# Performance work log

Measured on AMD Instinct MI355X. Metric: run time of the kernel, lower is better.

The kernel has to match this reference:

```python
import jax, jax.numpy as jnp
import numpy as np

B, S, D, H = 4, 2048, 1024, 16
DK = D // H


def setup_inputs() -> dict:
    key = jax.random.key(0)
    ks = jax.random.split(key, 12)
    s = 1.0 / np.sqrt(D)
    return {
        "query": jax.random.normal(ks[0], (B, S, D), jnp.float32),
        "key": jax.random.normal(ks[1], (B, S, D), jnp.float32),
        "value": jax.random.normal(ks[2], (B, S, D), jnp.float32),
        "mask": jax.random.randint(ks[3], (B, S), 0, 2, jnp.int32),
        "wq": jax.random.normal(ks[4], (D, D), jnp.float32) * s,
        "bq": jnp.zeros((D,), jnp.float32),
        "wk": jax.random.normal(ks[5], (D, D), jnp.float32) * s,
        "bk": jnp.zeros((D,), jnp.float32),
        "wv": jax.random.normal(ks[6], (D, D), jnp.float32) * s,
        "bv": jnp.zeros((D,), jnp.float32),
        "wo": jax.random.normal(ks[7], (D, D), jnp.float32) * s,
        "bo": jnp.zeros((D,), jnp.float32),
    }


def reference(query, key, value, mask, wq, bq, wk, bk, wv, bv, wo, bo):
    # torch Linear: y = x @ W.T + b
    def proj(x, w, b):
        y = jnp.einsum('bsd,ed->bse', x, w) + b
        return y.reshape(B, S, H, DK).transpose(0, 2, 1, 3)  # [B,H,S,DK]

    q = proj(query, wq, bq)
    k = proj(key, wk, bk)
    v = proj(value, wv, bv)

    scores = jnp.einsum('bhqd,bhkd->bhqk', q, k) / jnp.sqrt(jnp.float32(DK))
    m = mask[:, None, None, :]  # [B,1,1,S_kv]
    scores = jnp.where(m == 0, jnp.float32(-1e9), scores)
    attn = jax.nn.softmax(scores, axis=-1)  # dropout p=0.0 (eval)
    out = jnp.einsum('bhqk,bhkd->bhqd', attn, v)
    out = out.transpose(0, 2, 1, 3).reshape(B, S, D)
    return jnp.einsum('bsd,ed->bse', out, wo) + bo
```

## Files before the change

kernel.cpp:

```cpp
#include <hip/hip_runtime.h>
#include <hip/hip_bf16.h>

typedef __bf16 bf16;
typedef bf16 bf16x2 __attribute__((ext_vector_type(2)));
typedef bf16 bf16x4 __attribute__((ext_vector_type(4)));
typedef bf16 bf16x8 __attribute__((ext_vector_type(8)));
typedef float f32x4 __attribute__((ext_vector_type(4)));
typedef float f32x16 __attribute__((ext_vector_type(16)));
typedef unsigned int u32;
typedef u32 u32x4 __attribute__((ext_vector_type(4)));

#define MFMA16(A,B,C) __builtin_amdgcn_mfma_f32_16x16x32_bf16(A,B,C,0,0,0)
#define MFMA32(A,B,C) __builtin_amdgcn_mfma_f32_32x32x16_bf16(A,B,C,0,0,0)

__device__ __forceinline__ void gld_lds16(const void* g, void* l) {
  __builtin_amdgcn_global_load_lds(
      (const __attribute__((address_space(1))) void*)g,
      (__attribute__((address_space(3))) void*)l, 16, 0, 0);
}

__global__ void cast3_kernel(const float* __restrict__ s0, const float* __restrict__ s1,
                             const float* __restrict__ s2,
                             bf16* __restrict__ d0, bf16* __restrict__ d1, bf16* __restrict__ d2) {
  const int which = blockIdx.x >> 13;
  const int i = (blockIdx.x & 8191) * 256 + threadIdx.x;
  const float* s = which == 0 ? s0 : which == 1 ? s1 : s2;
  bf16* d = which == 0 ? d0 : which == 1 ? d1 : d2;
  float4 v = ((const float4*)s)[i];
  bf16x4 o;
  o[0] = (bf16)v.x; o[1] = (bf16)v.y; o[2] = (bf16)v.z; o[3] = (bf16)v.w;
  *(bf16x4*)(d + (size_t)i * 4) = o;
}

__global__ void cast4_kernel(const float* __restrict__ s0, const float* __restrict__ s1,
                             const float* __restrict__ s2, const float* __restrict__ s3,
                             bf16* __restrict__ d0, bf16* __restrict__ d1,
                             bf16* __restrict__ d2, bf16* __restrict__ d3) {
  const int which = blockIdx.x >> 10;
  const int i = (blockIdx.x & 1023) * 256 + threadIdx.x;
  const float* s = which == 0 ? s0 : which == 1 ? s1 : which == 2 ? s2 : s3;
  bf16* d = which == 0 ? d0 : which == 1 ? d1 : which == 2 ? d2 : d3;
  float4 v = ((const float4*)s)[i];
  bf16x4 o;
  o[0] = (bf16)v.x; o[1] = (bf16)v.y; o[2] = (bf16)v.z; o[3] = (bf16)v.w;
  *(bf16x4*)(d + (size_t)i * 4) = o;
}

__device__ __forceinline__ void gemm256_core(
    const bf16* __restrict__ aBase, const bf16* __restrict__ bBase,
    bf16* sA, bf16* sB, f32x4 (&acc)[4][4])
{
  const int t = threadIdx.x;
  const int lane = t & 63, w = t >> 6;
  const int wr = w >> 2, wc = w & 3;
  const int c = lane & 15, g = lane >> 4;

  const int pA = t * 16;
  const int lA = pA ^ (((pA >> 7) & 7) << 4);
  const int srA = lA >> 6;
  const int scA = (lA & 63) >> 1;

  auto stage = [&](int buf, int kt) {
    gld_lds16(aBase + (size_t)srA * 1024 + kt * 32 + scA, &sA[buf * 4096 + t * 8]);
#pragma unroll
    for (int r = 0; r < 2; ++r)
      gld_lds16(bBase + (size_t)(r * 128 + srA) * 1024 + kt * 32 + scA,
                &sB[buf * 8192 + r * 4096 + t * 8]);
  };

  auto rd = [&](const bf16* s, int row) -> bf16x8 {
    const int phys = (row * 64 + g * 16) ^ (((row >> 1) & 7) << 4);
    return *(const bf16x8*)((const char*)s + phys);
  };

  stage(0, 0);
  int buf = 0;
#pragma unroll 1
  for (int kt = 0; kt < 32; ++kt) {
    __builtin_amdgcn_s_barrier();
    if (kt < 31) {
      stage(buf ^ 1, kt + 1);
      asm volatile("s_waitcnt vmcnt(3)" ::: "memory");
    } else {
      asm volatile("s_waitcnt vmcnt(0)" ::: "memory");
    }
    __builtin_amdgcn_s_barrier();

    const bf16* tA = sA + buf * 4096;
    const bf16* tB = sB + buf * 8192;
    bf16x8 af[4], bfr[4];
#pragma unroll
    for (int mi = 0; mi < 4; ++mi) af[mi] = rd(tA, wr * 64 + mi * 16 + c);
#pragma unroll
    for (int ni = 0; ni < 4; ++ni) bfr[ni] = rd(tB, wc * 64 + ni * 16 + c);
    __builtin_amdgcn_s_setprio(1);
#pragma unroll
    for (int mi = 0; mi < 4; ++mi)
#pragma unroll
      for (int ni = 0; ni < 4; ++ni)
        acc[mi][ni] = MFMA16(af[mi], bfr[ni], acc[mi][ni]);
    __builtin_amdgcn_s_setprio(0);
    buf ^= 1;
  }
}

__global__ __launch_bounds__(512, 4) void qkv_gemm256(
    const bf16* __restrict__ qx, const bf16* __restrict__ kx, const bf16* __restrict__ vx,
    const bf16* __restrict__ wqb, const bf16* __restrict__ wkb, const bf16* __restrict__ wvb,
    const float* __restrict__ bq, const float* __restrict__ bk, const float* __restrict__ bv,
    bf16* __restrict__ qp, bf16* __restrict__ kp, bf16* __restrict__ vt, float qscale)
{
  __shared__ bf16 sA[2 * 4096];
  __shared__ bf16 sB[2 * 8192];
  const int z = blockIdx.z;
  const bf16* A   = z == 0 ? qx  : z == 1 ? kx  : vx;
  const bf16* Bm  = z == 0 ? wqb : z == 1 ? wkb : wvb;
  const float* bias = z == 0 ? bq : z == 1 ? bk : bv;
  const int bm = blockIdx.y, bn = blockIdx.x;

  f32x4 acc[4][4] = {};
  gemm256_core(A + (size_t)(bm * 128) * 1024, Bm + (size_t)(bn * 256) * 1024, sA, sB, acc);

  const int t = threadIdx.x, lane = t & 63, w = t >> 6;
  const int wr = w >> 2, wc = w & 3, c = lane & 15, g = lane >> 4;
  const float sc = z == 0 ? qscale : 1.0f;
  bf16* Cb = z == 0 ? qp : kp;
#pragma unroll
  for (int ni = 0; ni < 4; ++ni) {
    const int col = bn * 256 + wc * 64 + ni * 16 + c;
    const float bvv = bias[col];
#pragma unroll
    for (int mi = 0; mi < 4; ++mi) {
#pragma unroll
      for (int r4 = 0; r4 < 4; ++r4) {
        const int row = bm * 128 + wr * 64 + mi * 16 + g * 4 + r4;
        const float val = (acc[mi][ni][r4] + bvv) * sc;
        if (z == 2) {
          const int bb = row >> 11, s = row & 2047;
          vt[((size_t)(bb * 1024 + col)) * 2048 + s] = (bf16)val;
        } else {
          Cb[(size_t)row * 1024 + col] = (bf16)val;
        }
      }
    }
  }
}

__global__ __launch_bounds__(512, 4) void out_gemm256(
    const bf16* __restrict__ A, const bf16* __restrict__ Bm,
    const float* __restrict__ bias, float* __restrict__ Cout)
{
  __shared__ bf16 sA[2 * 4096];
  __shared__ bf16 sB[2 * 8192];
  const int bm = blockIdx.y, bn = blockIdx.x;

  f32x4 acc[4][4] = {};
  gemm256_core(A + (size_t)(bm * 128) * 1024, Bm + (size_t)(bn * 256) * 1024, sA, sB, acc);

  const int t = threadIdx.x, lane = t & 63, w = t >> 6;
  const int wr = w >> 2, wc = w & 3, c = lane & 15, g = lane >> 4;
#pragma unroll
  for (int ni = 0; ni < 4; ++ni) {
    const int col = bn * 256 + wc * 64 + ni * 16 + c;
    const float bvv = bias[col];
#pragma unroll
    for (int mi = 0; mi < 4; ++mi) {
#pragma unroll
      for (int r4 = 0; r4 < 4; ++r4) {
        const int row = bm * 128 + wr * 64 + mi * 16 + g * 4 + r4;
        Cout[(size_t)row * 1024 + col] = acc[mi][ni][r4] + bvv;
      }
    }
  }
}

__global__ __launch_bounds__(256) void attn_kernel(
    const bf16* __restrict__ Qp, const bf16* __restrict__ Kp, const bf16* __restrict__ Vt,
    const int* __restrict__ mask, bf16* __restrict__ Out)
{
  __shared__ bf16 sKV[2][64 * 128];

  const int bh = blockIdx.x;
  const int b = bh >> 4, h = bh & 15;
  const int t = threadIdx.x, lane = t & 63, w = t >> 6;
  const int q32 = lane & 31, hi = lane >> 5;
  const int q0 = blockIdx.y * 128 + w * 32;

  const char* kBase = (const char*)(Kp + (size_t)(b * 2048) * 1024 + h * 64);
  const char* vBase = (const char*)(Vt + (size_t)(bh * 64) * 2048);

  auto stageKV = [&](int buf, int kt) {
#pragma unroll
    for (int j = 0; j < 4; ++j) {
      const int P = j * 4096 + t * 16;
      const int L = P ^ (((P >> 8) & 15) << 4);
      const int row = L >> 8;
      const int off = L & 255;
      const char* src = (off < 128)
          ? kBase + (size_t)(kt * 64 + row) * 2048 + off
          : vBase + (size_t)row * 4096 + kt * 128 + (off - 128);
      gld_lds16(src, (char*)sKV[buf] + P);
    }
  };

  bf16x8 qf[4];
  const bf16* qrow = Qp + (size_t)(b * 2048 + q0 + q32) * 1024 + h * 64;
#pragma unroll
  for (int ks = 0; ks < 4; ++ks)
    qf[ks] = *(const bf16x8*)&qrow[ks * 16 + hi * 8];

  float mrun = -1e30f, lrun = 0.f;
  f32x16 aco[2] = {};

  const int* mrow = mask + b * 2048;

  stageKV(0, 0);
  __syncthreads();
  int cur = 0;
  for (int kt = 0; kt < 32; ++kt) {
    if (kt + 1 < 32) stageKV(cur ^ 1, kt + 1);

    f32x16 st[2];
#pragma unroll
    for (int kf = 0; kf < 2; ++kf)
#pragma unroll
      for (int q4 = 0; q4 < 4; ++q4) {
        const int4 mm = *(const int4*)&mrow[kt * 64 + kf * 32 + q4 * 8 + hi * 4];
        st[kf][q4 * 4 + 0] = mm.x ? 0.0f : -1e9f;
        st[kf][q4 * 4 + 1] = mm.y ? 0.0f : -1e9f;
        st[kf][q4 * 4 + 2] = mm.z ? 0.0f : -1e9f;
        st[kf][q4 * 4 + 3] = mm.w ? 0.0f : -1e9f;
      }

#pragma unroll
    for (int ks = 0; ks < 4; ++ks) {
      bf16x8 k0f, k1f;
      {
        const int row = q32;
        const int phys = row * 256 + ((ks * 32 + hi * 16) ^ ((row & 15) << 4));
        k0f = *(const bf16x8*)((const char*)sKV[cur] + phys);
      }
      {
        const int row = 32 + q32;
        const int phys = row * 256 + ((ks * 32 + hi * 16) ^ ((row & 15) << 4));
        k1f = *(const bf16x8*)((const char*)sKV[cur] + phys);
      }
      __builtin_amdgcn_s_setprio(1);
      st[0] = MFMA32(k0f, qf[ks], st[0]);
      st[1] = MFMA32(k1f, qf[ks], st[1]);
      __builtin_amdgcn_s_setprio(0);
    }

    float t0 = fmaxf(st[0][0], st[0][1]), t1 = fmaxf(st[0][2], st[0][3]);
    float t2 = fmaxf(st[1][0], st[1][1]), t3 = fmaxf(st[1][2], st[1][3]);
#pragma unroll
    for (int i = 4; i < 16; i += 4) {
      t0 = fmaxf(t0, fmaxf(st[0][i], st[0][i + 1]));
      t1 = fmaxf(t1, fmaxf(st[0][i + 2], st[0][i + 3]));
      t2 = fmaxf(t2, fmaxf(st[1][i], st[1][i + 1]));
      t3 = fmaxf(t3, fmaxf(st[1][i + 2], st[1][i + 3]));
    }
    float tmax = fmaxf(fmaxf(t0, t1), fmaxf(t2, t3));
    tmax = fmaxf(tmax, __shfl_xor(tmax, 32, 64));
    if (!__all(tmax <= mrun + 11.5f)) {
      const float mnew = fmaxf(mrun, tmax);
      const float sc = exp2f(mrun - mnew);
      mrun = mnew;
      lrun *= sc;
      aco[0] *= sc;
      aco[1] *= sc;
    }
    float rs0 = 0.f, rs1 = 0.f, rs2 = 0.f, rs3 = 0.f;
#pragma unroll
    for (int i = 0; i < 16; i += 4) {
      float p00 = exp2f(st[0][i] - mrun),     p01 = exp2f(st[0][i + 1] - mrun);
      float p02 = exp2f(st[0][i + 2] - mrun), p03 = exp2f(st[0][i + 3] - mrun);
      float p10 = exp2f(st[1][i] - mrun),     p11 = exp2f(st[1][i + 1] - mrun);
      float p12 = exp2f(st[1][i + 2] - mrun), p13 = exp2f(st[1][i + 3] - mrun);
      st[0][i] = p00; st[0][i + 1] = p01; st[0][i + 2] = p02; st[0][i + 3] = p03;
      st[1][i] = p10; st[1][i + 1] = p11; st[1][i + 2] = p12; st[1][i + 3] = p13;
      rs0 += p00 + p01; rs1 += p02 + p03;
      rs2 += p10 + p11; rs3 += p12 + p13;
    }
    float rs = (rs0 + rs1) + (rs2 + rs3);
    rs += __shfl_xor(rs, 32, 64);
    lrun += rs;

    bf16x8 pa[4];
#pragma unroll
    for (int kf = 0; kf < 2; ++kf) {
      u32 u[4][2];
#pragma unroll
      for (int g2 = 0; g2 < 4; ++g2) {
        asm("v_cvt_pk_bf16_f32 %0, %1, %2"
            : "=v"(u[g2][0]) : "v"(st[kf][4 * g2 + 0]), "v"(st[kf][4 * g2 + 1]));
        asm("v_cvt_pk_bf16_f32 %0, %1, %2"
            : "=v"(u[g2][1]) : "v"(st[kf][4 * g2 + 2]), "v"(st[kf][4 * g2 + 3]));
      }
      u32 d0 = u[0][0], d2 = u[1][0];
      asm("v_permlane32_swap_b32 %0, %1" : "+v"(d0), "+v"(d2));
      u32 d1 = u[0][1], d3 = u[1][1];
      asm("v_permlane32_swap_b32 %0, %1" : "+v"(d1), "+v"(d3));
      u32x4 ud = {d0, d1, d2, d3};
      pa[2 * kf] = __builtin_bit_cast(bf16x8, ud);
      u32 e0 = u[2][0], e2 = u[3][0];
      asm("v_permlane32_swap_b32 %0, %1" : "+v"(e0), "+v"(e2));
      u32 e1 = u[2][1], e3 = u[3][1];
      asm("v_permlane32_swap_b32 %0, %1" : "+v"(e1), "+v"(e3));
      u32x4 ue = {e0, e1, e2, e3};
      pa[2 * kf + 1] = __builtin_bit_cast(bf16x8, ue);
    }

#pragma unroll
    for (int kk = 0; kk < 4; ++kk) {
      bf16x8 vb0, vb1;
      {
        const int row = q32;
        const int phys = row * 256 + ((128 + kk * 32 + hi * 16) ^ ((row & 15) << 4));
        vb0 = *(const bf16x8*)((const char*)sKV[cur] + phys);
      }
      {
        const int row = 32 + q32;
        const int phys = row * 256 + ((128 + kk * 32 + hi * 16) ^ ((row & 15) << 4));
        vb1 = *(const bf16x8*)((const char*)sKV[cur] + phys);
      }
      __builtin_amdgcn_s_setprio(1);
      aco[0] = MFMA32(vb0, pa[kk], aco[0]);
      aco[1] = MFMA32(vb1, pa[kk], aco[1]);
      __builtin_amdgcn_s_setprio(0);
    }

    __syncthreads();
    cur ^= 1;
  }

  const float inv = 1.0f / lrun;
  bf16* orow = Out + (size_t)(b * 2048 + q0 + q32) * 1024 + h * 64;
#pragma unroll
  for (int dkf = 0; dkf < 2; ++dkf)
#pragma unroll
    for (int q4 = 0; q4 < 4; ++q4) {
      bf16x4 o;
#pragma unroll
      for (int r4 = 0; r4 < 4; ++r4)
        o[r4] = (bf16)(aco[dkf][q4 * 4 + r4] * inv);
      *(bf16x4*)&orow[dkf * 32 + q4 * 8 + hi * 4] = o;
    }
}

extern "C" void kernel_launch(void* const* d_in, const int* in_sizes, int n_in,
                              void* d_out, int out_size, void* d_ws, size_t ws_size,
                              hipStream_t stream) {
  const float* q  = (const float*)d_in[0];
  const float* k  = (const float*)d_in[1];
  const float* v  = (const float*)d_in[2];
  const int*  msk = (const int*)d_in[3];
  const float* wq = (const float*)d_in[4];
  const float* bq = (const float*)d_in[5];
  const float* wk = (const float*)d_in[6];
  const float* bk = (const float*)d_in[7];
  const float* wv = (const float*)d_in[8];
  const float* bv = (const float*)d_in[9];
  const float* wo = (const float*)d_in[10];
  const float* bo = (const float*)d_in[11];

  bf16* ws = (bf16*)d_ws;
  const size_t NEL = 8192ull * 1024ull;
  bf16* qx  = ws;
  bf16* kx  = ws + NEL;
  bf16* vx  = ws + 2 * NEL;
  bf16* wqb = ws + 3 * NEL;
  bf16* wkb = wqb + 1048576;
  bf16* wvb = wkb + 1048576;
  bf16* wob = wvb + 1048576;
  bf16* qp  = wob + 1048576;
  bf16* kp  = qp + NEL;
  bf16* vt  = kp + NEL;
  bf16* ao  = vx;

  cast3_kernel<<<24576, 256, 0, stream>>>(q, k, v, qx, kx, vx);
  cast4_kernel<<<4096, 256, 0, stream>>>(wq, wk, wv, wo, wqb, wkb, wvb, wob);

  const float qscale = 0.125f * 1.44269504088896f;
  qkv_gemm256<<<dim3(4, 64, 3), 512, 0, stream>>>(qx, kx, vx, wqb, wkb, wvb,
                                                  bq, bk, bv, qp, kp, vt, qscale);
  attn_kernel<<<dim3(64, 16), 256, 0, stream>>>(qp, kp, vt, msk, ao);
  out_gemm256<<<dim3(4, 64), 512, 0, stream>>>(ao, wob, bo, (float*)d_out);
}
```

Measured before the change: 467.2 us.

## Shrink GEMM tiles to 128x128, precompute float mask, use max3 reductions

Both projection GEMMs change from 128x256 tiles with 512 threads to 128x128 tiles with 256 threads. This doubles the grid size and halves the per-block B tile in LDS, trading some operand reuse for more blocks and better occupancy. A small kernel now converts the int mask to additive float values once, so the attention loop loads floats directly instead of selecting per element. The row-max reduction in attention is rewritten as chained three-way max calls so the compiler can emit 3-input max instructions.

```diff
diff --git a/kernel.cpp b/kernel.cpp
--- a/kernel.cpp
+++ b/kernel.cpp
@@ -17,6 +17,10 @@
   __builtin_amdgcn_global_load_lds(
       (const __attribute__((address_space(1))) void*)g,
       (__attribute__((address_space(3))) void*)l, 16, 0, 0);
+}
+
+__device__ __forceinline__ float max3f(float a, float b, float c) {
+  return fmaxf(fmaxf(a, b), c);
 }
 
 __global__ void cast3_kernel(const float* __restrict__ s0, const float* __restrict__ s1,
@@ -46,32 +50,51 @@
   *(bf16x4*)(d + (size_t)i * 4) = o;
 }
 
-__device__ __forceinline__ void gemm256_core(
+__global__ void maskf_kernel(const int* __restrict__ m, float* __restrict__ mf) {
+  const int i = blockIdx.x * 256 + threadIdx.x;
+  const int4 v = ((const int4*)m)[i];
+  float4 o;
+  o.x = v.x ? 0.0f : -1e9f;
+  o.y = v.y ? 0.0f : -1e9f;
+  o.z = v.z ? 0.0f : -1e9f;
+  o.w = v.w ? 0.0f : -1e9f;
+  ((float4*)mf)[i] = o;
+}
+
+__device__ __forceinline__ void gemm128_core(
     const bf16* __restrict__ aBase, const bf16* __restrict__ bBase,
     bf16* sA, bf16* sB, f32x4 (&acc)[4][4])
 {
   const int t = threadIdx.x;
   const int lane = t & 63, w = t >> 6;
-  const int wr = w >> 2, wc = w & 3;
   const int c = lane & 15, g = lane >> 4;
 
-  const int pA = t * 16;
-  const int lA = pA ^ (((pA >> 7) & 7) << 4);
-  const int srA = lA >> 6;
-  const int scA = (lA & 63) >> 1;
+  int srow[2], scol[2];
+#pragma unroll
+  for (int i = 0; i < 2; ++i) {
+    const int P = i * 4096 + t * 16;
+    const int L = P ^ (((P >> 7) & 7) << 4);
+    srow[i] = L >> 6;
+    scol[i] = (L & 63) >> 1;
+  }
 
   auto stage = [&](int buf, int kt) {
-    gld_lds16(aBase + (size_t)srA * 1024 + kt * 32 + scA, &sA[buf * 4096 + t * 8]);
-#pragma unroll
-    for (int r = 0; r < 2; ++r)
-      gld_lds16(bBase + (size_t)(r * 128 + srA) * 1024 + kt * 32 + scA,
-                &sB[buf * 8192 + r * 4096 + t * 8]);
+#pragma unroll
+    for (int i = 0; i < 2; ++i)
+      gld_lds16(aBase + (size_t)srow[i] * 1024 + kt * 32 + scol[i],
+                &sA[buf * 4096 + i * 2048 + t * 8]);
+#pragma unroll
+    for (int i = 0; i < 2; ++i)
+      gld_lds16(bBase + (size_t)srow[i] * 1024 + kt * 32 + scol[i],
+                &sB[buf * 4096 + i * 2048 + t * 8]);
   };
 
   auto rd = [&](const bf16* s, int row) -> bf16x8 {
     const int phys = (row * 64 + g * 16) ^ (((row >> 1) & 7) << 4);
     return *(const bf16x8*)((const char*)s + phys);
   };
+
+  const int wr = w >> 1, wc = w & 1;
 
   stage(0, 0);
   int buf = 0;
@@ -80,14 +103,14 @@
     __builtin_amdgcn_s_barrier();
     if (kt < 31) {
       stage(buf ^ 1, kt + 1);
-      asm volatile("s_waitcnt vmcnt(3)" ::: "memory");
+      asm volatile("s_waitcnt vmcnt(4)" ::: "memory");
     } else {
       asm volatile("s_waitcnt vmcnt(0)" ::: "memory");
     }
     __builtin_amdgcn_s_barrier();
 
     const bf16* tA = sA + buf * 4096;
-    const bf16* tB = sB + buf * 8192;
+    const bf16* tB = sB + buf * 4096;
     bf16x8 af[4], bfr[4];
 #pragma unroll
     for (int mi = 0; mi < 4; ++mi) af[mi] = rd(tA, wr * 64 + mi * 16 + c);
@@ -104,30 +127,30 @@
   }
 }
 
-__global__ __launch_bounds__(512, 4) void qkv_gemm256(
+__global__ __launch_bounds__(256) void qkv_gemm128(
     const bf16* __restrict__ qx, const bf16* __restrict__ kx, const bf16* __restrict__ vx,
     const bf16* __restrict__ wqb, const bf16* __restrict__ wkb, const bf16* __restrict__ wvb,
     const float* __restrict__ bq, const float* __restrict__ bk, const float* __restrict__ bv,
     bf16* __restrict__ qp, bf16* __restrict__ kp, bf16* __restrict__ vt, float qscale)
 {
   __shared__ bf16 sA[2 * 4096];
-  __shared__ bf16 sB[2 * 8192];
+  __shared__ bf16 sB[2 * 4096];
   const int z = blockIdx.z;
-  const bf16* A   = z == 0 ? qx  : z == 1 ? kx  : vx;
-  const bf16* Bm  = z == 0 ? wqb : z == 1 ? wkb : wvb;
+  const bf16* A    = z == 0 ? qx  : z == 1 ? kx  : vx;
+  const bf16* Bm   = z == 0 ? wqb : z == 1 ? wkb : wvb;
   const float* bias = z == 0 ? bq : z == 1 ? bk : bv;
   const int bm = blockIdx.y, bn = blockIdx.x;
 
   f32x4 acc[4][4] = {};
-  gemm256_core(A + (size_t)(bm * 128) * 1024, Bm + (size_t)(bn * 256) * 1024, sA, sB, acc);
+  gemm128_core(A + (size_t)(bm * 128) * 1024, Bm + (size_t)(bn * 128) * 1024, sA, sB, acc);
 
   const int t = threadIdx.x, lane = t & 63, w = t >> 6;
-  const int wr = w >> 2, wc = w & 3, c = lane & 15, g = lane >> 4;
+  const int wr = w >> 1, wc = w & 1, c = lane & 15, g = lane >> 4;
   const float sc = z == 0 ? qscale : 1.0f;
   bf16* Cb = z == 0 ? qp : kp;
 #pragma unroll
   for (int ni = 0; ni < 4; ++ni) {
-    const int col = bn * 256 + wc * 64 + ni * 16 + c;
+    const int col = bn * 128 + wc * 64 + ni * 16 + c;
     const float bvv = bias[col];
 #pragma unroll
     for (int mi = 0; mi < 4; ++mi) {
@@ -146,22 +169,22 @@
   }
 }
 
-__global__ __launch_bounds__(512, 4) void out_gemm256(
+__global__ __launch_bounds__(256) void out_gemm128(
     const bf16* __restrict__ A, const bf16* __restrict__ Bm,
     const float* __restrict__ bias, float* __restrict__ Cout)
 {
   __shared__ bf16 sA[2 * 4096];
-  __shared__ bf16 sB[2 * 8192];
+  __shared__ bf16 sB[2 * 4096];
   const int bm = blockIdx.y, bn = blockIdx.x;
 
   f32x4 acc[4][4] = {};
-  gemm256_core(A + (size_t)(bm * 128) * 1024, Bm + (size_t)(bn * 256) * 1024, sA, sB, acc);
+  gemm128_core(A + (size_t)(bm * 128) * 1024, Bm + (size_t)(bn * 128) * 1024, sA, sB, acc);
 
   const int t = threadIdx.x, lane = t & 63, w = t >> 6;
-  const int wr = w >> 2, wc = w & 3, c = lane & 15, g = lane >> 4;
+  const int wr = w >> 1, wc = w & 1, c = lane & 15, g = lane >> 4;
 #pragma unroll
   for (int ni = 0; ni < 4; ++ni) {
-    const int col = bn * 256 + wc * 64 + ni * 16 + c;
+    const int col = bn * 128 + wc * 64 + ni * 16 + c;
     const float bvv = bias[col];
 #pragma unroll
     for (int mi = 0; mi < 4; ++mi) {
@@ -176,7 +199,7 @@
 
 __global__ __launch_bounds__(256) void attn_kernel(
     const bf16* __restrict__ Qp, const bf16* __restrict__ Kp, const bf16* __restrict__ Vt,
-    const int* __restrict__ mask, bf16* __restrict__ Out)
+    const float* __restrict__ maskf, bf16* __restrict__ Out)
 {
   __shared__ bf16 sKV[2][64 * 128];
 
@@ -212,7 +235,7 @@
   float mrun = -1e30f, lrun = 0.f;
   f32x16 aco[2] = {};
 
-  const int* mrow = mask + b * 2048;
+  const float* mrow = maskf + b * 2048;
 
   stageKV(0, 0);
   __syncthreads();
@@ -225,11 +248,11 @@
     for (int kf = 0; kf < 2; ++kf)
 #pragma unroll
       for (int q4 = 0; q4 < 4; ++q4) {
-        const int4 mm = *(const int4*)&mrow[kt * 64 + kf * 32 + q4 * 8 + hi * 4];
-        st[kf][q4 * 4 + 0] = mm.x ? 0.0f : -1e9f;
-        st[kf][q4 * 4 + 1] = mm.y ? 0.0f : -1e9f;
-        st[kf][q4 * 4 + 2] = mm.z ? 0.0f : -1e9f;
-        st[kf][q4 * 4 + 3] = mm.w ? 0.0f : -1e9f;
+        const float4 mm = *(const float4*)&mrow[kt * 64 + kf * 32 + q4 * 8 + hi * 4];
+        st[kf][q4 * 4 + 0] = mm.x;
+        st[kf][q4 * 4 + 1] = mm.y;
+        st[kf][q4 * 4 + 2] = mm.z;
+        st[kf][q4 * 4 + 3] = mm.w;
       }
 
 #pragma unroll
@@ -251,16 +274,23 @@
       __builtin_amdgcn_s_setprio(0);
     }
 
-    float t0 = fmaxf(st[0][0], st[0][1]), t1 = fmaxf(st[0][2], st[0][3]);
-    float t2 = fmaxf(st[1][0], st[1][1]), t3 = fmaxf(st[1][2], st[1][3]);
-#pragma unroll
-    for (int i = 4; i < 16; i += 4) {
-      t0 = fmaxf(t0, fmaxf(st[0][i], st[0][i + 1]));
-      t1 = fmaxf(t1, fmaxf(st[0][i + 2], st[0][i + 3]));
-      t2 = fmaxf(t2, fmaxf(st[1][i], st[1][i + 1]));
-      t3 = fmaxf(t3, fmaxf(st[1][i + 2], st[1][i + 3]));
-    }
-    float tmax = fmaxf(fmaxf(t0, t1), fmaxf(t2, t3));
+    float c0 = max3f(st[0][0], st[0][1], st[0][2]);
+    c0 = max3f(c0, st[0][3], st[0][4]);
+    c0 = max3f(c0, st[0][5], st[0][6]);
+    c0 = fmaxf(c0, st[0][7]);
+    float c1 = max3f(st[0][8], st[0][9], st[0][10]);
+    c1 = max3f(c1, st[0][11], st[0][12]);
+    c1 = max3f(c1, st[0][13], st[0][14]);
+    c1 = fmaxf(c1, st[0][15]);
+    float c2 = max3f(st[1][0], st[1][1], st[1][2]);
+    c2 = max3f(c2, st[1][3], st[1][4]);
+    c2 = max3f(c2, st[1][5], st[1][6]);
+    c2 = fmaxf(c2, st[1][7]);
+    float c3 = max3f(st[1][8], st[1][9], st[1][10]);
+    c3 = max3f(c3, st[1][11], st[1][12]);
+    c3 = max3f(c3, st[1][13], st[1][14]);
+    c3 = fmaxf(c3, st[1][15]);
+    float tmax = fmaxf(max3f(c0, c1, c2), c3);
     tmax = fmaxf(tmax, __shfl_xor(tmax, 32, 64));
     if (!__all(tmax <= mrun + 11.5f)) {
       const float mnew = fmaxf(mrun, tmax);
@@ -376,14 +406,16 @@
   bf16* qp  = wob + 1048576;
   bf16* kp  = qp + NEL;
   bf16* vt  = kp + NEL;
+  float* mf = (float*)(vt + NEL);
   bf16* ao  = vx;
 
   cast3_kernel<<<24576, 256, 0, stream>>>(q, k, v, qx, kx, vx);
   cast4_kernel<<<4096, 256, 0, stream>>>(wq, wk, wv, wo, wqb, wkb, wvb, wob);
+  maskf_kernel<<<8, 256, 0, stream>>>(msk, mf);
 
   const float qscale = 0.125f * 1.44269504088896f;
-  qkv_gemm256<<<dim3(4, 64, 3), 512, 0, stream>>>(qx, kx, vx, wqb, wkb, wvb,
+  qkv_gemm128<<<dim3(8, 64, 3), 256, 0, stream>>>(qx, kx, vx, wqb, wkb, wvb,
                                                   bq, bk, bv, qp, kp, vt, qscale);
-  attn_kernel<<<dim3(64, 16), 256, 0, stream>>>(qp, kp, vt, msk, ao);
-  out_gemm256<<<dim3(4, 64), 512, 0, stream>>>(ao, wob, bo, (float*)d_out);
-}
+  attn_kernel<<<dim3(64, 16), 256, 0, stream>>>(qp, kp, vt, mf, ao);
+  out_gemm128<<<dim3(8, 64), 256, 0, stream>>>(ao, wob, bo, (float*)d_out);
+}
```

Result: faster. 435.3 us (-6.8%).
